# Optimization experiments

Measured on AMD Instinct MI355X. Metric: run time of the kernel, lower is better.

## Reference

```python
import jax, jax.numpy as jnp
import numpy as np

# Concrete segmented-polynomial instance (uniform 1d):
N = 8192      # nodes (rows of input 0 and of the indexed output)
E = 16384     # edges (batch dim of input 1 and of the per-edge product)
S = 16        # segments per operand (buffer_num_segments, same for all 3 operands)
EXT = 64      # operand_extent (uniform segment shape)
P = 2048      # num_paths of the single operation


def setup_inputs() -> dict:
    key = jax.random.key(0)
    k0, k1, k2, k3, k4, k5 = jax.random.split(key, 6)
    x = jax.random.normal(k0, (N, S * EXT), dtype=jnp.float32)          # node features
    y = jax.random.normal(k1, (E, S * EXT), dtype=jnp.float32)          # edge features
    idx_in = jax.random.randint(k2, (E,), 0, N, dtype=jnp.int32)        # gather index for input 0
    idx_out = jax.random.randint(k3, (E,), 0, N, dtype=jnp.int32)       # scatter index for output 0
    path_indices = jax.random.randint(k4, (P, 3), 0, S, dtype=jnp.int32)  # (i_x, j_y, k_out) per path
    path_coefficients = jax.random.normal(k5, (P,), dtype=jnp.float32)
    return {
        "x": x, "y": y,
        "idx_in": idx_in, "idx_out": idx_out,
        "path_indices": path_indices,
        "path_coefficients": path_coefficients,
    }


def reference(x, y, idx_in, idx_out, path_indices, path_coefficients):
    # Dense path-coefficient tensor C[k, i, j]: duplicate paths accumulate,
    # missing (k,i,j) triples are zero. This is the math-dtype (fp32) contraction
    # the uniform-1d kernel performs over segments of equal extent.
    C = jnp.zeros((S, S, S), dtype=x.dtype).at[
        path_indices[:, 2], path_indices[:, 0], path_indices[:, 1]
    ].add(path_coefficients)

    xr = x.reshape(N, S, EXT)[idx_in]   # gather (BATCH_DIM_INDEXED input): [E, S, EXT]
    yr = y.reshape(E, S, EXT)           # batched input:                    [E, S, EXT]

    # out_e[e, k, c] = sum_{i,j} C[k,i,j] * xr[e,i,c] * yr[e,j,c]
    out_e = jnp.einsum('kij,eic,ejc->ekc', C, xr, yr)

    # scatter-add (BATCH_DIM_INDEXED output) into N output rows
    out = jnp.zeros((N, S, EXT), dtype=x.dtype).at[idx_out].add(out_e)
    return out.reshape(N, S * EXT)
```

## Files before the change

### kernel.cpp

```cpp
#include <hip/hip_runtime.h>
#include <hip/hip_bf16.h>

#define N_NODES 8192
#define E_EDGES 16384
#define S_SEG   16
#define EXT     64
#define P_PATHS 2048
#define ROW     (S_SEG * EXT)

typedef _Float16 f16x8  __attribute__((ext_vector_type(8)));
typedef _Float16 half2v __attribute__((ext_vector_type(2)));
typedef float    f32x4  __attribute__((ext_vector_type(4)));

#define WS_CMAT  0
#define WS_HIST  8192
#define WS_CURS  40960
#define WS_ROWS  73728
#define WS_ELIST 106512

__global__ void prep(const int* __restrict__ pidx, const float* __restrict__ pcoef,
                     _Float16* __restrict__ Cmat, int* __restrict__ hist) {
    const int tid = threadIdx.x;
    if (blockIdx.x < 32) {
        hist[blockIdx.x * 256 + tid] = 0;
        return;
    }
    __shared__ float sC[S_SEG * S_SEG * S_SEG];
    for (int i = tid; i < 4096; i += 256) sC[i] = 0.f;
    __syncthreads();
    for (int p = tid; p < P_PATHS; p += 256) {
        int i = pidx[3 * p + 0];
        int j = pidx[3 * p + 1];
        int k = pidx[3 * p + 2];
        atomicAdd(&sC[(k * S_SEG + i) * S_SEG + j], pcoef[p]);
    }
    __syncthreads();
    for (int i = tid; i < 4096; i += 256) Cmat[i] = (_Float16)sC[i];
}

__global__ void hist_k(const int* __restrict__ idx_out, int* __restrict__ hist) {
    const int e = blockIdx.x * 256 + threadIdx.x;
    atomicAdd(&hist[idx_out[e]], 1);
}

__global__ __launch_bounds__(256) void scan_k(const int* __restrict__ hist,
                                              int* __restrict__ rows,
                                              int* __restrict__ cursor) {
    __shared__ int part[256];
    const int t = threadIdx.x;
    const int base = t * 32;
    int loc[32];
    int s = 0;
#pragma unroll
    for (int i = 0; i < 32; ++i) { loc[i] = s; s += hist[base + i]; }
    part[t] = s;
    __syncthreads();
    for (int off = 1; off < 256; off <<= 1) {
        int v = part[t];
        int u = (t >= off) ? part[t - off] : 0;
        __syncthreads();
        part[t] = v + u;
        __syncthreads();
    }
    const int excl = (t == 0) ? 0 : part[t - 1];
#pragma unroll
    for (int i = 0; i < 32; ++i) {
        int v = excl + loc[i];
        rows[base + i] = v;
        cursor[base + i] = v;
    }
    if (t == 255) rows[N_NODES] = part[255];
}

__global__ void scatter_k(const int* __restrict__ idx_out, int* __restrict__ cursor,
                          int* __restrict__ elist) {
    const int e = blockIdx.x * 256 + threadIdx.x;
    const int pos = atomicAdd(&cursor[idx_out[e]], 1);
    elist[pos] = e;
}

__global__ __launch_bounds__(256) void seg_poly_node(
        const float* __restrict__ x, const float* __restrict__ y,
        const int* __restrict__ idx_in, const _Float16* __restrict__ Cmat,
        const int* __restrict__ rows, const int* __restrict__ elist,
        float* __restrict__ out) {
    __shared__ __attribute__((aligned(16))) _Float16 sxh[ROW];
    __shared__ __attribute__((aligned(16))) half2v  syp[512];

    const int tid  = threadIdx.x;
    const int lane = tid & 63;
    const int wv   = tid >> 6;
    const int quad = lane >> 4;
    const int c    = wv * 16 + (lane & 15);
    const int n    = blockIdx.x;

    const int beg = rows[n];
    const int end = rows[n + 1];

    f16x8 afrag[8];
    {
        const _Float16* basep = Cmat + (lane & 15) * 256 + quad * 8;
#pragma unroll
        for (int kk = 0; kk < 8; ++kk)
            afrag[kk] = *(const f16x8*)(basep + kk * 32);
    }

    f32x4 acc = {0.f, 0.f, 0.f, 0.f};
    const int jb2 = (quad & 1) * 4;
    const int ih  = quad >> 1;

    for (int p = beg; p < end; ++p) {
        const int e  = elist[p];
        const int xr = idx_in[e];

        {
            const float4 xv = *(const float4*)(x + (size_t)xr * ROW + tid * 4);
            half2v* sxp = (half2v*)sxh;
            sxp[tid * 2]     = half2v{(_Float16)xv.x, (_Float16)xv.y};
            sxp[tid * 2 + 1] = half2v{(_Float16)xv.z, (_Float16)xv.w};
        }
        if (tid < 128) {
            const int jp = tid >> 4;
            const int cq = (tid & 15) * 4;
            const float* yb = y + (size_t)e * ROW;
            const float4 ya = *(const float4*)(yb + (2 * jp) * EXT + cq);
            const float4 yc = *(const float4*)(yb + (2 * jp + 1) * EXT + cq);
            syp[jp * 64 + cq + 0] = half2v{(_Float16)ya.x, (_Float16)yc.x};
            syp[jp * 64 + cq + 1] = half2v{(_Float16)ya.y, (_Float16)yc.y};
            syp[jp * 64 + cq + 2] = half2v{(_Float16)ya.z, (_Float16)yc.z};
            syp[jp * 64 + cq + 3] = half2v{(_Float16)ya.w, (_Float16)yc.w};
        }
        __syncthreads();

        half2v ypk[4];
#pragma unroll
        for (int r = 0; r < 4; ++r) ypk[r] = syp[(jb2 + r) * 64 + c];

#pragma unroll
        for (int kk = 0; kk < 8; ++kk) {
            const _Float16 xh = sxh[(2 * kk + ih) * EXT + c];
            const half2v hx = {xh, xh};
            const half2v b0 = hx * ypk[0];
            const half2v b1 = hx * ypk[1];
            const half2v b2 = hx * ypk[2];
            const half2v b3 = hx * ypk[3];
            const f16x8 bfrag = {b0[0], b0[1], b1[0], b1[1], b2[0], b2[1], b3[0], b3[1]};
            acc = __builtin_amdgcn_mfma_f32_16x16x32_f16(afrag[kk], bfrag, acc, 0, 0, 0);
        }
        __syncthreads();
    }

    float* ob = out + (size_t)n * ROW;
#pragma unroll
    for (int r = 0; r < 4; ++r)
        ob[(quad * 4 + r) * EXT + c] = acc[r];
}

extern "C" void kernel_launch(void* const* d_in, const int* in_sizes, int n_in,
                              void* d_out, int out_size, void* d_ws, size_t ws_size,
                              hipStream_t stream) {
    const float* x       = (const float*)d_in[0];
    const float* y       = (const float*)d_in[1];
    const int*   idx_in  = (const int*)d_in[2];
    const int*   idx_out = (const int*)d_in[3];
    const int*   pidx    = (const int*)d_in[4];
    const float* pcoef   = (const float*)d_in[5];
    float* out           = (float*)d_out;

    char* ws = (char*)d_ws;
    _Float16* Cmat = (_Float16*)(ws + WS_CMAT);
    int* hist      = (int*)(ws + WS_HIST);
    int* cursor    = (int*)(ws + WS_CURS);
    int* rows      = (int*)(ws + WS_ROWS);
    int* elist     = (int*)(ws + WS_ELIST);

    prep<<<33, 256, 0, stream>>>(pidx, pcoef, Cmat, hist);
    hist_k<<<E_EDGES / 256, 256, 0, stream>>>(idx_out, hist);
    scan_k<<<1, 256, 0, stream>>>(hist, rows, cursor);
    scatter_k<<<E_EDGES / 256, 256, 0, stream>>>(idx_out, cursor, elist);
    seg_poly_node<<<N_NODES, 256, 0, stream>>>(x, y, idx_in, Cmat, rows, elist, out);
}
```

Before: 169.3 us.

## Assign one node per wavefront instead of one node per block

The per-node kernel now gives each wavefront its own node, with a private LDS slice, and each wave handles all four 16-column tiles itself. This removes the block-wide __syncthreads barriers in every edge iteration and lets waves progress independently. The trade-offs are a 4x larger LDS footprint per block, more accumulator registers, and load imbalance within a block when nodes have different degrees. Each wave also now serializes loads and MFMAs over its edges.

```diff
diff --git a/kernel.cpp b/kernel.cpp
--- a/kernel.cpp
+++ b/kernel.cpp
@@ -9,6 +9,7 @@
 #define ROW     (S_SEG * EXT)
 
 typedef _Float16 f16x8  __attribute__((ext_vector_type(8)));
+typedef _Float16 f16x4  __attribute__((ext_vector_type(4)));
 typedef _Float16 half2v __attribute__((ext_vector_type(2)));
 typedef float    f32x4  __attribute__((ext_vector_type(4)));
 
@@ -79,81 +80,98 @@
     elist[pos] = e;
 }
 
-__global__ __launch_bounds__(256) void seg_poly_node(
+__global__ __launch_bounds__(256) void seg_poly_wave(
         const float* __restrict__ x, const float* __restrict__ y,
         const int* __restrict__ idx_in, const _Float16* __restrict__ Cmat,
         const int* __restrict__ rows, const int* __restrict__ elist,
         float* __restrict__ out) {
-    __shared__ __attribute__((aligned(16))) _Float16 sxh[ROW];
-    __shared__ __attribute__((aligned(16))) half2v  syp[512];
+    __shared__ __attribute__((aligned(16))) _Float16 sx_all[4][ROW];
+    __shared__ __attribute__((aligned(16))) half2v   sy_all[4][512];
 
     const int tid  = threadIdx.x;
     const int lane = tid & 63;
     const int wv   = tid >> 6;
-    const int quad = lane >> 4;
-    const int c    = wv * 16 + (lane & 15);
-    const int n    = blockIdx.x;
-
+    _Float16* sxh = sx_all[wv];
+    half2v*   syp = sy_all[wv];
+
+    const int n = blockIdx.x * 4 + wv;
     const int beg = rows[n];
     const int end = rows[n + 1];
 
+    const int quad = lane >> 4;
+    const int m    = lane & 15;
+    const int jb2  = (quad & 1) * 4;
+    const int ih   = quad >> 1;
+
     f16x8 afrag[8];
     {
-        const _Float16* basep = Cmat + (lane & 15) * 256 + quad * 8;
+        const _Float16* basep = Cmat + m * 256 + quad * 8;
 #pragma unroll
         for (int kk = 0; kk < 8; ++kk)
             afrag[kk] = *(const f16x8*)(basep + kk * 32);
     }
 
-    f32x4 acc = {0.f, 0.f, 0.f, 0.f};
-    const int jb2 = (quad & 1) * 4;
-    const int ih  = quad >> 1;
+    f32x4 acc[4];
+#pragma unroll
+    for (int ct = 0; ct < 4; ++ct) acc[ct] = f32x4{0.f, 0.f, 0.f, 0.f};
 
     for (int p = beg; p < end; ++p) {
         const int e  = elist[p];
         const int xr = idx_in[e];
 
         {
-            const float4 xv = *(const float4*)(x + (size_t)xr * ROW + tid * 4);
-            half2v* sxp = (half2v*)sxh;
-            sxp[tid * 2]     = half2v{(_Float16)xv.x, (_Float16)xv.y};
-            sxp[tid * 2 + 1] = half2v{(_Float16)xv.z, (_Float16)xv.w};
+            const float* xb = x + (size_t)xr * ROW;
+#pragma unroll
+            for (int k4 = 0; k4 < 4; ++k4) {
+                const float4 v = *(const float4*)(xb + k4 * 256 + lane * 4);
+                f16x4 h = {(_Float16)v.x, (_Float16)v.y, (_Float16)v.z, (_Float16)v.w};
+                *(f16x4*)(sxh + k4 * 256 + lane * 4) = h;
+            }
         }
-        if (tid < 128) {
-            const int jp = tid >> 4;
-            const int cq = (tid & 15) * 4;
+        {
+            const int jp = lane >> 3;
+            const int cq = (lane & 7) * 8;
             const float* yb = y + (size_t)e * ROW;
-            const float4 ya = *(const float4*)(yb + (2 * jp) * EXT + cq);
-            const float4 yc = *(const float4*)(yb + (2 * jp + 1) * EXT + cq);
-            syp[jp * 64 + cq + 0] = half2v{(_Float16)ya.x, (_Float16)yc.x};
-            syp[jp * 64 + cq + 1] = half2v{(_Float16)ya.y, (_Float16)yc.y};
-            syp[jp * 64 + cq + 2] = half2v{(_Float16)ya.z, (_Float16)yc.z};
-            syp[jp * 64 + cq + 3] = half2v{(_Float16)ya.w, (_Float16)yc.w};
+            const float4 a0 = *(const float4*)(yb + (2 * jp)     * EXT + cq);
+            const float4 a1 = *(const float4*)(yb + (2 * jp)     * EXT + cq + 4);
+            const float4 b0 = *(const float4*)(yb + (2 * jp + 1) * EXT + cq);
+            const float4 b1 = *(const float4*)(yb + (2 * jp + 1) * EXT + cq + 4);
+            f16x8 p0 = {(_Float16)a0.x, (_Float16)b0.x, (_Float16)a0.y, (_Float16)b0.y,
+                        (_Float16)a0.z, (_Float16)b0.z, (_Float16)a0.w, (_Float16)b0.w};
+            f16x8 p1 = {(_Float16)a1.x, (_Float16)b1.x, (_Float16)a1.y, (_Float16)b1.y,
+                        (_Float16)a1.z, (_Float16)b1.z, (_Float16)a1.w, (_Float16)b1.w};
+            *(f16x8*)(syp + jp * 64 + cq)     = p0;
+            *(f16x8*)(syp + jp * 64 + cq + 4) = p1;
         }
-        __syncthreads();
-
-        half2v ypk[4];
-#pragma unroll
-        for (int r = 0; r < 4; ++r) ypk[r] = syp[(jb2 + r) * 64 + c];
-
-#pragma unroll
-        for (int kk = 0; kk < 8; ++kk) {
-            const _Float16 xh = sxh[(2 * kk + ih) * EXT + c];
-            const half2v hx = {xh, xh};
-            const half2v b0 = hx * ypk[0];
-            const half2v b1 = hx * ypk[1];
-            const half2v b2 = hx * ypk[2];
-            const half2v b3 = hx * ypk[3];
-            const f16x8 bfrag = {b0[0], b0[1], b1[0], b1[1], b2[0], b2[1], b3[0], b3[1]};
-            acc = __builtin_amdgcn_mfma_f32_16x16x32_f16(afrag[kk], bfrag, acc, 0, 0, 0);
+
+#pragma unroll
+        for (int ct = 0; ct < 4; ++ct) {
+            const int c = ct * 16 + m;
+            half2v ypk[4];
+#pragma unroll
+            for (int r = 0; r < 4; ++r) ypk[r] = syp[(jb2 + r) * 64 + c];
+#pragma unroll
+            for (int kk = 0; kk < 8; ++kk) {
+                const _Float16 xh = sxh[(2 * kk + ih) * EXT + c];
+                const half2v hx = {xh, xh};
+                const half2v b0 = hx * ypk[0];
+                const half2v b1 = hx * ypk[1];
+                const half2v b2 = hx * ypk[2];
+                const half2v b3 = hx * ypk[3];
+                const f16x8 bfrag = {b0[0], b0[1], b1[0], b1[1],
+                                     b2[0], b2[1], b3[0], b3[1]};
+                acc[ct] = __builtin_amdgcn_mfma_f32_16x16x32_f16(
+                              afrag[kk], bfrag, acc[ct], 0, 0, 0);
+            }
         }
-        __syncthreads();
     }
 
     float* ob = out + (size_t)n * ROW;
 #pragma unroll
-    for (int r = 0; r < 4; ++r)
-        ob[(quad * 4 + r) * EXT + c] = acc[r];
+    for (int ct = 0; ct < 4; ++ct)
+#pragma unroll
+        for (int r = 0; r < 4; ++r)
+            ob[(quad * 4 + r) * EXT + ct * 16 + m] = acc[ct][r];
 }
 
 extern "C" void kernel_launch(void* const* d_in, const int* in_sizes, int n_in,
@@ -178,5 +196,5 @@
     hist_k<<<E_EDGES / 256, 256, 0, stream>>>(idx_out, hist);
     scan_k<<<1, 256, 0, stream>>>(hist, rows, cursor);
     scatter_k<<<E_EDGES / 256, 256, 0, stream>>>(idx_out, cursor, elist);
-    seg_poly_node<<<N_NODES, 256, 0, stream>>>(x, y, idx_in, Cmat, rows, elist, out);
-}
+    seg_poly_wave<<<N_NODES / 4, 256, 0, stream>>>(x, y, idx_in, Cmat, rows, elist, out);
+}
```

Result: faster. 165.6 us (-2.2%).
